# Optimization experiments

Hardware: AMD Instinct MI355X
Metric: run time of the kernel (lower is better)

The kernel has to match this reference:

```python
import jax, jax.numpy as jnp
import numpy as np

B, N_IN, N_HID, N_OUT = 4096, 1024, 4096, 1024

def setup_inputs() -> dict:
    key = jax.random.key(0)
    k_x, k_w1, k_b1, k_w2, k_b2 = jax.random.split(key, 5)
    # Per-node LiveNet weights, batched: each hidden neuron = relu(sum_i w_i * in_i + b),
    # each output neuron = linear sum over hidden neurons.
    s1 = 1.0 / np.sqrt(N_IN)
    s2 = 1.0 / np.sqrt(N_HID)
    return {
        "x": jax.random.normal(k_x, (B, N_IN), dtype=jnp.float32),
        "W1": jax.random.uniform(k_w1, (N_IN, N_HID), jnp.float32, -s1, s1),
        "b1": jax.random.uniform(k_b1, (N_HID,), jnp.float32, -s1, s1),
        "W2": jax.random.uniform(k_w2, (N_HID, N_OUT), jnp.float32, -s2, s2),
        "b2": jax.random.uniform(k_b2, (N_OUT,), jnp.float32, -s2, s2),
    }

def reference(x, W1, b1, W2, b2):
    # Batched equivalent of LiveNet's per-node traversal:
    # inputs[i].set_output(x[:, i:i+1]); each hidden neuron computes
    # relu(weighted sum of parents + bias); each output node is a linear
    # weighted sum of hidden outputs; outputs concatenated along dim=1.
    h = jax.nn.relu(x @ W1 + b1)          # [B, N_HID]
    y = h @ W2 + b2                        # [B, N_OUT]
    return y
```

## Files before the change

### kernel.cpp

```cpp
#include <hip/hip_runtime.h>
#include <stdint.h>

#define BDIM  4096
#define NIN   1024
#define NHID  4096
#define NOUT  1024

typedef unsigned short u16;
typedef unsigned int   u32;
typedef __attribute__((ext_vector_type(8))) __bf16 bf16x8;
typedef __attribute__((ext_vector_type(4))) float  f32x4;

__device__ __forceinline__ u16 f32_to_bf16_rne(float f) {
    u32 u = __builtin_bit_cast(u32, f);
    u = (u + 0x7fffu + ((u >> 16) & 1u)) >> 16;
    return (u16)u;
}
__device__ __forceinline__ float bf16_to_f32(u16 h) {
    u32 u = ((u32)h) << 16;
    return __builtin_bit_cast(float, u);
}

__device__ __forceinline__ void transpose_tile(
    const float* __restrict__ in, u16* __restrict__ out,
    int R, int C, int bx, int by, float (*tile)[33]) {
    const int rt = by * 32, ct = bx * 32;
    const int tid = threadIdx.x;
    {
        const int r  = tid >> 3;
        const int c4 = (tid & 7) * 4;
        float4 v = *(const float4*)(in + (size_t)(rt + r) * C + ct + c4);
        tile[r][c4 + 0] = v.x; tile[r][c4 + 1] = v.y;
        tile[r][c4 + 2] = v.z; tile[r][c4 + 3] = v.w;
    }
    __syncthreads();
    if (tid < 128) {
        const int oc = tid >> 2;
        const int ch = tid & 3;
        u16 tmp[8];
#pragma unroll
        for (int j = 0; j < 8; ++j)
            tmp[j] = f32_to_bf16_rne(tile[ch * 8 + j][oc]);
        u16* dst = out + (size_t)(ct + oc) * R + rt + ch * 8;
        ushort4 lo = {tmp[0], tmp[1], tmp[2], tmp[3]};
        ushort4 hi = {tmp[4], tmp[5], tmp[6], tmp[7]};
        *(ushort4*)dst = lo;
        *(ushort4*)(dst + 4) = hi;
    }
}

__global__ void prepass(const float* __restrict__ x,  u16* __restrict__ x_bf,
                        const float* __restrict__ W1, u16* __restrict__ W1t,
                        const float* __restrict__ W2, u16* __restrict__ W2t) {
    __shared__ float tile[32][33];
    const int b = blockIdx.x;
    if (b < 4096) {
        int i = b * 256 + threadIdx.x;
        float4 v = ((const float4*)x)[i];
        ushort4 o;
        o.x = f32_to_bf16_rne(v.x); o.y = f32_to_bf16_rne(v.y);
        o.z = f32_to_bf16_rne(v.z); o.w = f32_to_bf16_rne(v.w);
        ((ushort4*)x_bf)[i] = o;
    } else if (b < 8192) {
        int t = b - 4096;
        transpose_tile(W1, W1t, NIN, NHID, t & 127, t >> 7, tile);
    } else {
        int t = b - 8192;
        transpose_tile(W2, W2t, NHID, NOUT, t & 31, t >> 5, tile);
    }
}

__global__ __launch_bounds__(512) void gemm_bt_relu(
    const u16* __restrict__ A, const u16* __restrict__ Bt,
    const float* __restrict__ bias, u16* __restrict__ outp,
    int M, int N, int K)
{
    constexpr int MI = 4, NI = 4;
    __shared__ __align__(16) u16 smemA[256 * 64];
    __shared__ __align__(16) u16 smemB[128 * 64];

    const int bid = blockIdx.x;
    const int cxcd = bid & 7;
    const int j    = bid >> 3;
    const int bx   = ((cxcd & 3) << 3) + (j & 7);
    const int by   = ((cxcd >> 2) << 3) + (j >> 3);

    const int tid  = threadIdx.x;
    const int lane = tid & 63;
    const int wave = tid >> 6;
    const int rowBase = by * 256;
    const int colBase = bx * 128;
    const int wrow = (wave >> 1) * 64;
    const int wcol = (wave & 1) * 64;

    f32x4 acc[MI][NI] = {};

    const int srow    = lane >> 3;
    const int chunkSw = (lane & 7) ^ srow;
    const int gcol    = chunkSw * 8;
    const int fr = lane & 15;
    const int fq = lane >> 4;
    const int sw = fr & 7;

    for (int k0 = 0; k0 < K; k0 += 64) {
        __syncthreads();
#pragma unroll
        for (int t = 0; t < 4; ++t) {
            int region = wave * 4 + t;
            int arow = rowBase + region * 8 + srow;
            const u16* g = A + (size_t)arow * K + k0 + gcol;
            __builtin_amdgcn_global_load_lds(
                (const __attribute__((address_space(1))) u32*)g,
                (__attribute__((address_space(3))) u32*)(smemA + region * 512),
                16, 0, 0);
        }
#pragma unroll
        for (int t = 0; t < 2; ++t) {
            int region = wave * 2 + t;
            int brow = colBase + region * 8 + srow;
            const u16* g = Bt + (size_t)brow * K + k0 + gcol;
            __builtin_amdgcn_global_load_lds(
                (const __attribute__((address_space(1))) u32*)g,
                (__attribute__((address_space(3))) u32*)(smemB + region * 512),
                16, 0, 0);
        }
        __builtin_amdgcn_s_waitcnt(0);
        __syncthreads();

#pragma unroll
        for (int s = 0; s < 2; ++s) {
            const int co = ((s * 4 + fq) ^ sw) * 16;
            const char* aB = (const char*)smemA + (wrow + fr) * 128 + co;
            const char* bB = (const char*)smemB + (wcol + fr) * 128 + co;
            bf16x8 af[MI], bfv[NI];
#pragma unroll
            for (int mi = 0; mi < MI; ++mi)
                af[mi] = *(const bf16x8*)(aB + mi * 2048);
#pragma unroll
            for (int ni = 0; ni < NI; ++ni)
                bfv[ni] = *(const bf16x8*)(bB + ni * 2048);
#pragma unroll
            for (int mi = 0; mi < MI; ++mi)
#pragma unroll
                for (int ni = 0; ni < NI; ++ni)
                    acc[mi][ni] = __builtin_amdgcn_mfma_f32_16x16x32_bf16(
                        af[mi], bfv[ni], acc[mi][ni], 0, 0, 0);
        }
    }

    const int col0 = colBase + wcol + fr;
    const int row0 = rowBase + wrow + (fq << 2);
#pragma unroll
    for (int ni = 0; ni < NI; ++ni) {
        const int col = col0 + ni * 16;
        const float bv = bias[col];
#pragma unroll
        for (int mi = 0; mi < MI; ++mi) {
            const int row = row0 + mi * 16;
#pragma unroll
            for (int r = 0; r < 4; ++r) {
                float v = acc[mi][ni][r] + bv;
                v = v > 0.f ? v : 0.f;
                outp[(size_t)(row + r) * N + col] = f32_to_bf16_rne(v);
            }
        }
    }
}

__global__ __launch_bounds__(512) void gemm2_splitk(
    const u16* __restrict__ A, const u16* __restrict__ Bt,
    u16* __restrict__ pbf, int M, int N, int K, int Kchunk)
{
    constexpr int MI = 4, NI = 4;
    __shared__ __align__(16) u16 smemA[256 * 64];
    __shared__ __align__(16) u16 smemB[128 * 64];

    const int bid = blockIdx.x;
    const int cxcd = bid & 7;
    const int j    = bid >> 3;
    const int z    = cxcd >> 1;
    const int bx   = j & 7;
    const int by   = ((cxcd & 1) << 3) + (j >> 3);

    const int tid  = threadIdx.x;
    const int lane = tid & 63;
    const int wave = tid >> 6;
    const int rowBase = by * 256;
    const int colBase = bx * 128;
    const int kBeg = z * Kchunk;
    const int kEnd = kBeg + Kchunk;
    const int wrow = (wave >> 1) * 64;
    const int wcol = (wave & 1) * 64;

    f32x4 acc[MI][NI] = {};

    const int srow    = lane >> 3;
    const int chunkSw = (lane & 7) ^ srow;
    const int gcol    = chunkSw * 8;
    const int fr = lane & 15;
    const int fq = lane >> 4;
    const int sw = fr & 7;

    for (int k0 = kBeg; k0 < kEnd; k0 += 64) {
        __syncthreads();
#pragma unroll
        for (int t = 0; t < 4; ++t) {
            int region = wave * 4 + t;
            int arow = rowBase + region * 8 + srow;
            const u16* g = A + (size_t)arow * K + k0 + gcol;
            __builtin_amdgcn_global_load_lds(
                (const __attribute__((address_space(1))) u32*)g,
                (__attribute__((address_space(3))) u32*)(smemA + region * 512),
                16, 0, 0);
        }
#pragma unroll
        for (int t = 0; t < 2; ++t) {
            int region = wave * 2 + t;
            int brow = colBase + region * 8 + srow;
            const u16* g = Bt + (size_t)brow * K + k0 + gcol;
            __builtin_amdgcn_global_load_lds(
                (const __attribute__((address_space(1))) u32*)g,
                (__attribute__((address_space(3))) u32*)(smemB + region * 512),
                16, 0, 0);
        }
        __builtin_amdgcn_s_waitcnt(0);
        __syncthreads();

#pragma unroll
        for (int s = 0; s < 2; ++s) {
            const int co = ((s * 4 + fq) ^ sw) * 16;
            const char* aB = (const char*)smemA + (wrow + fr) * 128 + co;
            const char* bB = (const char*)smemB + (wcol + fr) * 128 + co;
            bf16x8 af[MI], bfv[NI];
#pragma unroll
            for (int mi = 0; mi < MI; ++mi)
                af[mi] = *(const bf16x8*)(aB + mi * 2048);
#pragma unroll
            for (int ni = 0; ni < NI; ++ni)
                bfv[ni] = *(const bf16x8*)(bB + ni * 2048);
#pragma unroll
            for (int mi = 0; mi < MI; ++mi)
#pragma unroll
                for (int ni = 0; ni < NI; ++ni)
                    acc[mi][ni] = __builtin_amdgcn_mfma_f32_16x16x32_bf16(
                        af[mi], bfv[ni], acc[mi][ni], 0, 0, 0);
        }
    }

    u16* outp = pbf + (size_t)z * M * N;
    const int col0 = colBase + wcol + fr;
    const int row0 = rowBase + wrow + (fq << 2);
#pragma unroll
    for (int ni = 0; ni < NI; ++ni) {
        const int col = col0 + ni * 16;
#pragma unroll
        for (int mi = 0; mi < MI; ++mi) {
            const int row = row0 + mi * 16;
#pragma unroll
            for (int r = 0; r < 4; ++r)
                outp[(size_t)(row + r) * N + col] =
                    f32_to_bf16_rne(acc[mi][ni][r]);
        }
    }
}

__global__ void splitk_reduce(float* __restrict__ out0,
                              const u16* __restrict__ pbf,
                              const float* __restrict__ bias,
                              int n4, int nCols4) {
    int i = blockIdx.x * blockDim.x + threadIdx.x;
    if (i >= n4) return;
    const size_t MN = (size_t)n4 * 4;
    float4 v = ((const float4*)bias)[i & (nCols4 - 1)];
#pragma unroll
    for (int s = 0; s < 4; ++s) {
        ushort4 q = ((const ushort4*)(pbf + s * MN))[i];
        v.x += bf16_to_f32(q.x); v.y += bf16_to_f32(q.y);
        v.z += bf16_to_f32(q.z); v.w += bf16_to_f32(q.w);
    }
    ((float4*)out0)[i] = v;
}

extern "C" void kernel_launch(void* const* d_in, const int* in_sizes, int n_in,
                              void* d_out, int out_size, void* d_ws, size_t ws_size,
                              hipStream_t stream) {
    const float* x  = (const float*)d_in[0];
    const float* W1 = (const float*)d_in[1];
    const float* b1 = (const float*)d_in[2];
    const float* W2 = (const float*)d_in[3];
    const float* b2 = (const float*)d_in[4];

    char* ws = (char*)d_ws;
    const size_t MB = 1024 * 1024;
    u16* W2t  = (u16*)(ws + 0 * MB);
    u16* h_bf = (u16*)(ws + 8 * MB);
    u16* x_bf = (u16*)(ws + 40 * MB);
    u16* W1t  = (u16*)(ws + 48 * MB);
    u16* pbf  = (u16*)(ws + 56 * MB);

    prepass<<<12288, 256, 0, stream>>>(x, x_bf, W1, W1t, W2, W2t);

    gemm_bt_relu<<<512, 512, 0, stream>>>(
        x_bf, W1t, b1, h_bf, BDIM, NHID, NIN);

    gemm2_splitk<<<512, 512, 0, stream>>>(
        h_bf, W2t, pbf, BDIM, NOUT, NHID, NHID / 4);

    int rn4 = BDIM * NOUT / 4;
    splitk_reduce<<<(rn4 + 255) / 256, 256, 0, stream>>>(
        (float*)d_out, pbf, b2, rn4, NOUT / 4);
}
```

Baseline: 171.7 us.

## Fuse split-K reduction into GEMM2 via last-arriving block with atomic counter

Removes the separate split-K reduce kernel. Each GEMM2 block writes its bf16 partial, then increments a per-tile atomic counter, and the last of the four K-slices sums the other partials with its own fp32 accumulator plus bias and writes the output. This saves one launch and the extra read of the partial buffer. It adds a memset launch and atomics, and the final reduction is done by a quarter of the blocks with strided, uncoalesced scalar loads.

```diff
diff --git a/kernel.cpp b/kernel.cpp
--- a/kernel.cpp
+++ b/kernel.cpp
@@ -169,11 +169,14 @@
 
 __global__ __launch_bounds__(512) void gemm2_splitk(
     const u16* __restrict__ A, const u16* __restrict__ Bt,
-    u16* __restrict__ pbf, int M, int N, int K, int Kchunk)
+    const float* __restrict__ bias, u16* __restrict__ pbf,
+    float* __restrict__ out0, u32* __restrict__ cnt,
+    int M, int N, int K, int Kchunk)
 {
     constexpr int MI = 4, NI = 4;
     __shared__ __align__(16) u16 smemA[256 * 64];
     __shared__ __align__(16) u16 smemB[128 * 64];
+    __shared__ int lastFlag;
 
     const int bid = blockIdx.x;
     const int cxcd = bid & 7;
@@ -247,9 +250,11 @@
         }
     }
 
-    u16* outp = pbf + (size_t)z * M * N;
+    const size_t MN = (size_t)M * N;
+    u16* myp = pbf + (size_t)z * MN;
     const int col0 = colBase + wcol + fr;
     const int row0 = rowBase + wrow + (fq << 2);
+
 #pragma unroll
     for (int ni = 0; ni < NI; ++ni) {
         const int col = col0 + ni * 16;
@@ -258,27 +263,37 @@
             const int row = row0 + mi * 16;
 #pragma unroll
             for (int r = 0; r < 4; ++r)
-                outp[(size_t)(row + r) * N + col] =
+                myp[(size_t)(row + r) * N + col] =
                     f32_to_bf16_rne(acc[mi][ni][r]);
         }
     }
-}
-
-__global__ void splitk_reduce(float* __restrict__ out0,
-                              const u16* __restrict__ pbf,
-                              const float* __restrict__ bias,
-                              int n4, int nCols4) {
-    int i = blockIdx.x * blockDim.x + threadIdx.x;
-    if (i >= n4) return;
-    const size_t MN = (size_t)n4 * 4;
-    float4 v = ((const float4*)bias)[i & (nCols4 - 1)];
-#pragma unroll
-    for (int s = 0; s < 4; ++s) {
-        ushort4 q = ((const ushort4*)(pbf + s * MN))[i];
-        v.x += bf16_to_f32(q.x); v.y += bf16_to_f32(q.y);
-        v.z += bf16_to_f32(q.z); v.w += bf16_to_f32(q.w);
-    }
-    ((float4*)out0)[i] = v;
+
+    __threadfence();
+    __syncthreads();
+    if (tid == 0)
+        lastFlag = (int)atomicAdd(&cnt[by * 8 + bx], 1u);
+    __syncthreads();
+    if (lastFlag != 3) return;
+
+    __threadfence();
+#pragma unroll
+    for (int ni = 0; ni < NI; ++ni) {
+        const int col = col0 + ni * 16;
+        const float bv = bias[col];
+#pragma unroll
+        for (int mi = 0; mi < MI; ++mi) {
+            const int row = row0 + mi * 16;
+#pragma unroll
+            for (int r = 0; r < 4; ++r) {
+                const size_t idx = (size_t)(row + r) * N + col;
+                float v = acc[mi][ni][r] + bv;
+#pragma unroll
+                for (int zz = 0; zz < 4; ++zz)
+                    if (zz != z) v += bf16_to_f32(pbf[zz * MN + idx]);
+                out0[idx] = v;
+            }
+        }
+    }
 }
 
 extern "C" void kernel_launch(void* const* d_in, const int* in_sizes, int n_in,
@@ -297,6 +312,9 @@
     u16* x_bf = (u16*)(ws + 40 * MB);
     u16* W1t  = (u16*)(ws + 48 * MB);
     u16* pbf  = (u16*)(ws + 56 * MB);
+    u32* cnt  = (u32*)(ws + 88 * MB);
+
+    hipMemsetAsync(cnt, 0, 128 * sizeof(u32), stream);
 
     prepass<<<12288, 256, 0, stream>>>(x, x_bf, W1, W1t, W2, W2t);
 
@@ -304,9 +322,5 @@
         x_bf, W1t, b1, h_bf, BDIM, NHID, NIN);
 
     gemm2_splitk<<<512, 512, 0, stream>>>(
-        h_bf, W2t, pbf, BDIM, NOUT, NHID, NHID / 4);
-
-    int rn4 = BDIM * NOUT / 4;
-    splitk_reduce<<<(rn4 + 255) / 256, 256, 0, stream>>>(
-        (float*)d_out, pbf, b2, rn4, NOUT / 4);
-}
+        h_bf, W2t, b2, pbf, (float*)d_out, cnt, BDIM, NOUT, NHID, NHID / 4);
+}
```

Result: slower. 502.2 us (+192.4%).
